# Kernel optimization log

Measured on AMD Instinct MI355X. Metric: run time of the kernel, lower is better.

## Reference

```python
import jax, jax.numpy as jnp
import numpy as np

B, T, D, H = 4, 1024, 512, 8
DK = D // H
P = 2 * T - 1  # relative position length


def rel_shift(x):
    # x: (b, h, t, 2t-1) -> (b, h, t, t), Transformer-XL relative shift
    b, h, t, p = x.shape
    x = jnp.pad(x, ((0, 0), (0, 0), (0, 0), (1, 0)))  # (b,h,t,p+1)
    x = x.reshape(b, h, p + 1, t)[:, :, 1:, :].reshape(b, h, t, p)
    return x[..., :t]


def setup_inputs() -> dict:
    key = jax.random.key(0)
    ks = jax.random.split(key, 16)
    s = 0.02
    return {
        "q": jax.random.normal(ks[0], (B, T, D), jnp.float32),
        "k": jax.random.normal(ks[1], (B, T, D), jnp.float32),
        "v": jax.random.normal(ks[2], (B, T, D), jnp.float32),
        "pos_emb": jax.random.normal(ks[3], (1, P, D), jnp.float32),
        "Wq": jax.random.normal(ks[4], (D, D), jnp.float32) * s,
        "bq": jnp.zeros((D,), jnp.float32),
        "Wk": jax.random.normal(ks[5], (D, D), jnp.float32) * s,
        "bk": jnp.zeros((D,), jnp.float32),
        "Wv": jax.random.normal(ks[6], (D, D), jnp.float32) * s,
        "bv": jnp.zeros((D,), jnp.float32),
        "Wp": jax.random.normal(ks[7], (D, D), jnp.float32) * s,
        "pos_bias_u": jax.random.normal(ks[8], (H, DK), jnp.float32) * s,
        "pos_bias_v": jax.random.normal(ks[9], (H, DK), jnp.float32) * s,
        "Wo": jax.random.normal(ks[10], (D, D), jnp.float32) * s,
        "bo": jnp.zeros((D,), jnp.float32),
    }


def reference(q, k, v, pos_emb, Wq, bq, Wk, bk, Wv, bv, Wp,
              pos_bias_u, pos_bias_v, Wo, bo):
    b, t, d = q.shape
    # QKV projections, split heads -> (b, t, h, dk)
    qh = (q @ Wq.T + bq).reshape(b, t, H, DK)
    kh = (k @ Wk.T + bk).reshape(b, t, H, DK)
    vh = (v @ Wv.T + bv).reshape(b, t, H, DK)
    # positional projection (no bias): (1, P, h, dk)
    ph = (pos_emb @ Wp.T).reshape(pos_emb.shape[1], H, DK)
    # content term: (q + u) . k
    q_u = qh + pos_bias_u  # (b,t,h,dk)
    matrix_ac = jnp.einsum("bqhd,bkhd->bhqk", q_u, kh)
    # position term: (q + v) . p, then relative shift
    q_v = qh + pos_bias_v
    matrix_bd = jnp.einsum("bqhd,phd->bhqp", q_v, ph)
    matrix_bd = rel_shift(matrix_bd)  # (b,h,t,t)
    scores = (matrix_ac + matrix_bd) / jnp.sqrt(jnp.float32(DK))
    attn = jax.nn.softmax(scores, axis=-1)
    out = jnp.einsum("bhqk,bkhd->bqhd", attn, vh).reshape(b, t, d)
    return out @ Wo.T + bo
```

## Files before the change

kernel.cpp:

```cpp
#include <hip/hip_runtime.h>
#include <math.h>

typedef unsigned short u16;
typedef _Float16 f16;
typedef __attribute__((ext_vector_type(8))) _Float16 f16x8;
typedef __attribute__((ext_vector_type(4))) float f32x4;

#define B_  4
#define T_  1024
#define D_  512
#define H_  8
#define DK_ 64
#define P_  2047

#define MFMAH(a, b, c) __builtin_amdgcn_mfma_f32_16x16x32_f16(a, b, c, 0, 0, 0)

__device__ __forceinline__ u16 f2hbits(float x) {
    union { f16 h; u16 u; } cv; cv.h = (f16)x; return cv.u;
}

__device__ __forceinline__ void gload_lds16(const u16* g, u16* l) {
    __builtin_amdgcn_global_load_lds(
        (const __attribute__((address_space(1))) void*)g,
        (__attribute__((address_space(3))) void*)l, 16, 0, 0);
}

__device__ __forceinline__ int swz8(int row, int colbase) {
    return row * 64 + (((colbase >> 3) ^ (row & 7)) << 3);
}

__global__ __launch_bounds__(256)
void conv_w(const float* __restrict__ wq, const float* __restrict__ wk,
            const float* __restrict__ wv, const float* __restrict__ wp,
            const float* __restrict__ wo,
            u16* wqs, u16* wks, u16* wvs, u16* wps, u16* wos)
{
    const int NW = 65536;
    int i = blockIdx.x * 256 + threadIdx.x;
    if (i >= 5 * NW) return;
    int which = i >> 16, off = i & (NW - 1);
    const float* src = which == 0 ? wq : which == 1 ? wk : which == 2 ? wv
                     : which == 3 ? wp : wo;
    u16* dst = which == 0 ? wqs : which == 1 ? wks : which == 2 ? wvs
             : which == 3 ? wps : wos;
    float4 x = *(const float4*)(src + (size_t)off * 4);
    union { f16 h[4]; uint2 u2; } cv;
    cv.h[0] = (f16)x.x; cv.h[1] = (f16)x.y;
    cv.h[2] = (f16)x.z; cv.h[3] = (f16)x.w;
    *(uint2*)(dst + (size_t)off * 4) = cv.u2;
}

__device__ __forceinline__ void gemm_core_f32(
    const float* __restrict__ A, const u16* __restrict__ Bw,
    int bm, int bn, int M, f32x4 (&acc)[4][4],
    u16 (&sA)[128][64], u16 (&sB)[128][64])
{
    const int tid = threadIdx.x;
    const int ln = tid & 63, w = tid >> 6;
    const int arow = ln & 15, kseg = ln >> 4;
    const int wr = w >> 1, wc = w & 1;

    for (int k0 = 0; k0 < 512; k0 += 64) {
        #pragma unroll
        for (int it = 0; it < 4; ++it) {
            int idx = it * 256 + tid;
            int r = idx >> 3, ch = idx & 7;
            int rm = bm + r; if (rm > M - 1) rm = M - 1;
            const float* s = A + (size_t)rm * 512 + k0 + ch * 8;
            float4 x = *(const float4*)s;
            float4 y = *(const float4*)(s + 4);
            union { f16 h[8]; f16x8 v; } pk;
            pk.h[0] = (f16)x.x; pk.h[1] = (f16)x.y;
            pk.h[2] = (f16)x.z; pk.h[3] = (f16)x.w;
            pk.h[4] = (f16)y.x; pk.h[5] = (f16)y.y;
            pk.h[6] = (f16)y.z; pk.h[7] = (f16)y.w;
            *(f16x8*)(&sA[r][(ch ^ (r & 7)) << 3]) = pk.v;
        }
        #pragma unroll
        for (int it = 0; it < 4; ++it) {
            int ch = it * 256 + tid;
            int r = ch >> 3, j = ch & 7;
            gload_lds16(Bw + (size_t)(bn + r) * 512 + k0 + ((j ^ (r & 7)) << 3),
                        &sB[0][0] + ch * 8);
        }
        __syncthreads();

        f16x8 af[4][2], bf[4][2];
        #pragma unroll
        for (int mi = 0; mi < 4; ++mi) {
            int row = wr * 64 + mi * 16 + arow;
            #pragma unroll
            for (int kc = 0; kc < 2; ++kc)
                af[mi][kc] = *(const f16x8*)
                    (&sA[row][0] + ((((kc << 2) | kseg) ^ (row & 7)) << 3));
        }
        #pragma unroll
        for (int nj = 0; nj < 4; ++nj) {
            int row = wc * 64 + nj * 16 + arow;
            #pragma unroll
            for (int kc = 0; kc < 2; ++kc)
                bf[nj][kc] = *(const f16x8*)
                    (&sB[row][0] + ((((kc << 2) | kseg) ^ (row & 7)) << 3));
        }
        #pragma unroll
        for (int mi = 0; mi < 4; ++mi)
            #pragma unroll
            for (int nj = 0; nj < 4; ++nj)
                #pragma unroll
                for (int kc = 0; kc < 2; ++kc)
                    acc[mi][nj] = MFMAH(af[mi][kc], bf[nj][kc], acc[mi][nj]);
        __syncthreads();
    }
}

__device__ __forceinline__ void gemm_core(
    const u16* __restrict__ A, const u16* __restrict__ Bw,
    int bm, int bn, int M, f32x4 (&acc)[4][4],
    u16 (&sA)[128][64], u16 (&sB)[128][64])
{
    const int tid = threadIdx.x;
    const int ln = tid & 63, w = tid >> 6;
    const int arow = ln & 15, kseg = ln >> 4;
    const int wr = w >> 1, wc = w & 1;

    for (int k0 = 0; k0 < 512; k0 += 64) {
        #pragma unroll
        for (int it = 0; it < 4; ++it) {
            int ch = it * 256 + tid;
            int r = ch >> 3, j = ch & 7;
            int rm = bm + r; if (rm > M - 1) rm = M - 1;
            gload_lds16(A + (size_t)rm * 512 + k0 + ((j ^ (r & 7)) << 3),
                        &sA[0][0] + ch * 8);
        }
        #pragma unroll
        for (int it = 0; it < 4; ++it) {
            int ch = it * 256 + tid;
            int r = ch >> 3, j = ch & 7;
            gload_lds16(Bw + (size_t)(bn + r) * 512 + k0 + ((j ^ (r & 7)) << 3),
                        &sB[0][0] + ch * 8);
        }
        __syncthreads();

        f16x8 af[4][2], bf[4][2];
        #pragma unroll
        for (int mi = 0; mi < 4; ++mi) {
            int row = wr * 64 + mi * 16 + arow;
            #pragma unroll
            for (int kc = 0; kc < 2; ++kc)
                af[mi][kc] = *(const f16x8*)
                    (&sA[row][0] + ((((kc << 2) | kseg) ^ (row & 7)) << 3));
        }
        #pragma unroll
        for (int nj = 0; nj < 4; ++nj) {
            int row = wc * 64 + nj * 16 + arow;
            #pragma unroll
            for (int kc = 0; kc < 2; ++kc)
                bf[nj][kc] = *(const f16x8*)
                    (&sB[row][0] + ((((kc << 2) | kseg) ^ (row & 7)) << 3));
        }
        #pragma unroll
        for (int mi = 0; mi < 4; ++mi)
            #pragma unroll
            for (int nj = 0; nj < 4; ++nj)
                #pragma unroll
                for (int kc = 0; kc < 2; ++kc)
                    acc[mi][nj] = MFMAH(af[mi][kc], bf[nj][kc], acc[mi][nj]);
        __syncthreads();
    }
}

__global__ __launch_bounds__(256, 3)
void gemm_qkvp(const float* __restrict__ q, const float* __restrict__ k,
               const float* __restrict__ v, const float* __restrict__ pe,
               const u16* __restrict__ wqs, const u16* __restrict__ wks,
               const u16* __restrict__ wvs, const u16* __restrict__ wps,
               const float* __restrict__ bq, const float* __restrict__ bk,
               const float* __restrict__ bv,
               const float* __restrict__ pbu, const float* __restrict__ pbv,
               u16* __restrict__ qub, u16* __restrict__ qvb,
               u16* __restrict__ kh, u16* __restrict__ vt, u16* __restrict__ ph)
{
    __shared__ u16 sA[128][64];
    __shared__ u16 sB[128][64];

    const int by = blockIdx.y;
    const float* A; const u16* Bw; const float* bias;
    int seg, bm, M, Tn;
    if (by < 32)      { seg=0; bm=by*128;       A=q;  Bw=wqs; bias=bq;      M=4096; Tn=T_; }
    else if (by < 64) { seg=1; bm=(by-32)*128;  A=k;  Bw=wks; bias=bk;      M=4096; Tn=T_; }
    else if (by < 96) { seg=2; bm=(by-64)*128;  A=v;  Bw=wvs; bias=bv;      M=4096; Tn=T_; }
    else              { seg=3; bm=(by-96)*128;  A=pe; Bw=wps; bias=nullptr; M=P_;   Tn=P_; }
    const int bn = blockIdx.x * 128;

    f32x4 acc[4][4] = {};
    gemm_core_f32(A, Bw, bm, bn, M, acc, sA, sB);

    const int tid = threadIdx.x;
    const int ln = tid & 63, w = tid >> 6;
    const int arow = ln & 15, kseg = ln >> 4;
    const int wr = w >> 1, wc = w & 1;

    float bv0[4];
    #pragma unroll
    for (int nj = 0; nj < 4; ++nj)
        bv0[nj] = bias ? bias[bn + wc * 64 + nj * 16 + arow] : 0.f;

    #pragma unroll
    for (int mi = 0; mi < 4; ++mi)
        #pragma unroll
        for (int r = 0; r < 4; ++r) {
            int m = bm + wr * 64 + mi * 16 + kseg * 4 + r;
            if (m >= M) continue;
            #pragma unroll
            for (int nj = 0; nj < 4; ++nj) {
                int n = bn + wc * 64 + nj * 16 + arow;
                float val = acc[mi][nj][r] + bv0[nj];
                if (seg == 0) {
                    int bb = m >> 10, t = m & 1023;
                    int hh = n >> 6, d = n & 63;
                    size_t off = ((size_t)(bb * H_ + hh) * T_ + t) * 64 + d;
                    qub[off] = f2hbits((val + pbu[hh * 64 + d]) * 0.125f);
                    qvb[off] = f2hbits((val + pbv[hh * 64 + d]) * 0.125f);
                } else if (seg == 2) {
                    int bb = m >> 10, t = m & 1023;
                    int hh = n >> 6, d = n & 63;
                    vt[((size_t)(bb * H_ + hh) * 64 + d) * T_ + t] = f2hbits(val);
                } else {
                    int bb = (Tn == T_) ? (m >> 10) : 0;
                    int t = m - bb * Tn;
                    int hh = n >> 6, d = n & 63;
                    size_t off = ((size_t)(bb * H_ + hh) * Tn + t) * 64 + d;
                    if (seg == 1) kh[off] = f2hbits(val);
                    else          ph[off] = f2hbits(val);
                }
            }
        }
}

__global__ __launch_bounds__(256, 3)
void gemm_out(const u16* __restrict__ A, const u16* __restrict__ Bw,
              const float* __restrict__ bias, float* __restrict__ C)
{
    __shared__ u16 sA[128][64];
    __shared__ u16 sB[128][64];
    const int bn = blockIdx.x * 128;
    const int bm = blockIdx.y * 128;
    f32x4 acc[4][4] = {};
    gemm_core(A, Bw, bm, bn, 4096, acc, sA, sB);

    const int tid = threadIdx.x;
    const int ln = tid & 63, w = tid >> 6;
    const int arow = ln & 15, kseg = ln >> 4;
    const int wr = w >> 1, wc = w & 1;
    #pragma unroll
    for (int mi = 0; mi < 4; ++mi)
        #pragma unroll
        for (int r = 0; r < 4; ++r) {
            int m = bm + wr * 64 + mi * 16 + kseg * 4 + r;
            #pragma unroll
            for (int nj = 0; nj < 4; ++nj) {
                int n = bn + wc * 64 + nj * 16 + arow;
                C[(size_t)m * 512 + n] = acc[mi][nj][r] + bias[n];
            }
        }
}

__global__ __launch_bounds__(256, 2)
void relattn_mfma(const u16* __restrict__ qub, const u16* __restrict__ qvb,
                  const u16* __restrict__ kh, const u16* __restrict__ vt,
                  const u16* __restrict__ ph,
                  u16* __restrict__ ao)
{
    __shared__ u16 s_k[3][64][64];
    __shared__ u16 s_p[3][64][64];
    __shared__ u16 s_pp[4][16][64];

    const int tid = threadIdx.x;
    const int ln  = tid & 63;
    const int w   = tid >> 6;
    const int arow = ln & 15;
    const int kseg = ln >> 4;

    const int lg = ((blockIdx.x & 7) << 6) | (blockIdx.x >> 3);
    const int qt = lg & 15, h = (lg >> 4) & 7, b = lg >> 7;
    const int q0 = qt * 64;

    const size_t kvbase = (size_t)(b * H_ + h) * T_ * 64;
    const size_t vtbase = (size_t)(b * H_ + h) * 64 * T_;
    const size_t pbase  = (size_t)h * P_ * 64;
    const int jb0 = 960 - q0;

    f16x8 qu[2], qv[2];
    {
        const u16* qb = qub + kvbase + (size_t)(q0 + w * 16 + arow) * 64;
        const u16* vb = qvb + kvbase + (size_t)(q0 + w * 16 + arow) * 64;
        #pragma unroll
        for (int c = 0; c < 2; ++c) {
            qu[c] = *(const f16x8*)(qb + c * 32 + kseg * 8);
            qv[c] = *(const f16x8*)(vb + c * 32 + kseg * 8);
        }
    }

    f32x4 o_[4] = {};
    float l_run[4] = {};

    auto stage_k = [&](int kt, int slot) {
        #pragma unroll
        for (int it = 0; it < 2; ++it) {
            int idx = tid + it * 256;
            int r = idx >> 3, ch = idx & 7;
            const u16* src = kh + kvbase + (size_t)(kt * 64 + r) * 64 + ((ch ^ (r & 7)) << 3);
            gload_lds16(src, &s_k[slot][0][0] + idx * 8);
        }
    };
    auto stage_p = [&](int c, int slot) {
        #pragma unroll
        for (int it = 0; it < 2; ++it) {
            int idx = tid + it * 256;
            int r = idx >> 3, ch = idx & 7;
            int j = jb0 + c * 64 + r; if (j > P_ - 1) j = P_ - 1;
            const u16* src = ph + pbase + (size_t)j * 64 + ((ch ^ (r & 7)) << 3);
            gload_lds16(src, &s_p[slot][0][0] + idx * 8);
        }
    };
    auto bd_chunk = [&](int slot, f32x4* out) {
        #pragma unroll
        for (int nb = 0; nb < 4; ++nb) {
            int pr = nb * 16 + arow;
            f16x8 b0 = *(const f16x8*)(&s_p[slot][0][0] + swz8(pr, kseg * 8));
            f16x8 b1 = *(const f16x8*)(&s_p[slot][0][0] + swz8(pr, 32 + kseg * 8));
            out[nb] = MFMAH(qv[0], b0, out[nb]);
            out[nb] = MFMAH(qv[1], b1, out[nb]);
        }
    };

    stage_k(0, 0); stage_k(1, 1);
    stage_p(0, 0); stage_p(1, 1); stage_p(2, 2);
    __syncthreads();
    f32x4 carry[4] = {};
    bd_chunk(0, carry);
    asm volatile("" ::: "memory");
    __builtin_amdgcn_s_barrier();
    asm volatile("" ::: "memory");

    int ks = 0;
    for (int t = 0; t < 16; ++t) {
        const int k0 = t * 64;
        const int pr = (ks + 1 > 2) ? 0 : ks + 1;
        const int kw = (ks + 2 > 2) ? ks - 1 : ks + 2;

        f16x8 vfr[4][2];
        #pragma unroll
        for (int nt = 0; nt < 4; ++nt) {
            const u16* vp = vt + vtbase + (size_t)(nt * 16 + arow) * T_ + k0 + kseg * 8;
            vfr[nt][0] = *(const f16x8*)vp;
            vfr[nt][1] = *(const f16x8*)(vp + 32);
        }

        if (t < 14) { stage_k(t + 2, kw); stage_p(t + 3, ks); }

        __builtin_amdgcn_s_setprio(1);
        f32x4 ac[4] = {};
        #pragma unroll
        for (int nt = 0; nt < 4; ++nt) {
            int kr = nt * 16 + arow;
            f16x8 b0 = *(const f16x8*)(&s_k[ks][0][0] + swz8(kr, kseg * 8));
            f16x8 b1 = *(const f16x8*)(&s_k[ks][0][0] + swz8(kr, 32 + kseg * 8));
            ac[nt] = MFMAH(qu[0], b0, ac[nt]);
            ac[nt] = MFMAH(qu[1], b1, ac[nt]);
        }
        f32x4 bdn[4] = {};
        bd_chunk(pr, bdn);
        __builtin_amdgcn_s_setprio(0);

        float win[5][4];
        #pragma unroll
        for (int r = 0; r < 4; ++r) {
            if (w == 0)      { win[0][r]=carry[3][r]; win[1][r]=bdn[0][r];   win[2][r]=bdn[1][r];   win[3][r]=bdn[2][r];   win[4][r]=bdn[3][r]; }
            else if (w == 1) { win[0][r]=carry[2][r]; win[1][r]=carry[3][r]; win[2][r]=bdn[0][r];   win[3][r]=bdn[1][r];   win[4][r]=bdn[2][r]; }
            else if (w == 2) { win[0][r]=carry[1][r]; win[1][r]=carry[2][r]; win[2][r]=carry[3][r]; win[3][r]=bdn[0][r];   win[4][r]=bdn[1][r]; }
            else             { win[0][r]=carry[0][r]; win[1][r]=carry[1][r]; win[2][r]=carry[2][r]; win[3][r]=carry[3][r]; win[4][r]=bdn[0][r]; }
        }

        #pragma unroll
        for (int r = 0; r < 4; ++r) {
            int sl  = 15 - (kseg << 2) - r;
            int src = (ln & 48) | ((arow + sl) & 15);
            bool hi = (arow < sl);
            int r16 = kseg * 4 + r;
            #pragma unroll
            for (int nt = 0; nt < 4; ++nt) {
                float sel = hi ? win[nt + 1][r] : win[nt][r];
                float pm = __shfl(sel, src, 64);
                float pv = __expf(ac[nt][r] + pm);
                l_run[r] += pv;
                int kl = nt * 16 + arow;
                s_pp[w][r16][(((kl >> 3) ^ (r16 & 7)) << 3) | (kl & 7)] = f2hbits(pv);
            }
        }
        asm volatile("s_waitcnt lgkmcnt(0)" ::: "memory");
        __builtin_amdgcn_sched_barrier(0);

        f16x8 pa0 = *(const f16x8*)(&s_pp[w][arow][0] + ((kseg ^ (arow & 7)) << 3));
        f16x8 pa1 = *(const f16x8*)(&s_pp[w][arow][0] + (((4 + kseg) ^ (arow & 7)) << 3));
        __builtin_amdgcn_s_setprio(1);
        #pragma unroll
        for (int nt = 0; nt < 4; ++nt) {
            o_[nt] = MFMAH(pa0, vfr[nt][0], o_[nt]);
            o_[nt] = MFMAH(pa1, vfr[nt][1], o_[nt]);
        }
        __builtin_amdgcn_s_setprio(0);

        #pragma unroll
        for (int nb = 0; nb < 4; ++nb) carry[nb] = bdn[nb];

        asm volatile("" ::: "memory");
        __builtin_amdgcn_s_barrier();
        asm volatile("" ::: "memory");
        ks = pr;
    }

    #pragma unroll
    for (int r = 0; r < 4; ++r) {
        float l = l_run[r];
        l += __shfl_xor(l, 1); l += __shfl_xor(l, 2);
        l += __shfl_xor(l, 4); l += __shfl_xor(l, 8);
        l_run[r] = 1.f / l;
    }
    #pragma unroll
    for (int nt = 0; nt < 4; ++nt)
        #pragma unroll
        for (int r = 0; r < 4; ++r) {
            int qrow = q0 + w * 16 + kseg * 4 + r;
            size_t off = ((size_t)(b * T_ + qrow)) * D_ + h * DK_ + nt * 16 + arow;
            ao[off] = f2hbits(o_[nt][r] * l_run[r]);
        }
}

extern "C" void kernel_launch(void* const* d_in, const int* in_sizes, int n_in,
                              void* d_out, int out_size, void* d_ws, size_t ws_size,
                              hipStream_t stream)
{
    const float* q   = (const float*)d_in[0];
    const float* k   = (const float*)d_in[1];
    const float* v   = (const float*)d_in[2];
    const float* pe  = (const float*)d_in[3];
    const float* Wq  = (const float*)d_in[4];
    const float* bq  = (const float*)d_in[5];
    const float* Wk  = (const float*)d_in[6];
    const float* bk  = (const float*)d_in[7];
    const float* Wv  = (const float*)d_in[8];
    const float* bv  = (const float*)d_in[9];
    const float* Wp  = (const float*)d_in[10];
    const float* pbu = (const float*)d_in[11];
    const float* pbv = (const float*)d_in[12];
    const float* Wo  = (const float*)d_in[13];
    const float* bo  = (const float*)d_in[14];
    float* out = (float*)d_out;

    char* ws = (char*)d_ws;
    const size_t MB = 1024 * 1024;
    const size_t HMB = 512 * 1024;
    u16* wqs = (u16*)(ws);
    u16* wks = (u16*)(ws + 1 * HMB);
    u16* wvs = (u16*)(ws + 2 * HMB);
    u16* wps = (u16*)(ws + 3 * HMB);
    u16* wos = (u16*)(ws + 4 * HMB);
    u16* qub = (u16*)(ws + 3 * MB);
    u16* qvb = (u16*)(ws + 7 * MB);
    u16* kh  = (u16*)(ws + 11 * MB);
    u16* vt  = (u16*)(ws + 15 * MB);
    u16* ph  = (u16*)(ws + 19 * MB);
    u16* ao  = (u16*)(ws + 22 * MB);

    dim3 blk(256);
    conv_w<<<dim3(1280), blk, 0, stream>>>(Wq, Wk, Wv, Wp, Wo,
                                           wqs, wks, wvs, wps, wos);

    gemm_qkvp<<<dim3(4, 112), blk, 0, stream>>>(
        q, k, v, pe, wqs, wks, wvs, wps,
        bq, bk, bv, pbu, pbv, qub, qvb, kh, vt, ph);

    relattn_mfma<<<dim3(512), blk, 0, stream>>>(qub, qvb, kh, vt, ph, ao);

    gemm_out<<<dim3(4, 32), blk, 0, stream>>>(ao, wos, bo, out);
}
```

Baseline: 93.05 us.

## Double-buffer LDS in projection GEMMs to overlap global loads with MFMA

Both GEMM cores switch to two LDS buffers so the next k-tile's global loads (register-staged fp32 A with f16 conversion, or direct-to-LDS for f16 operands) are issued before the current tile's MFMAs. Explicit waitcnt and s_barrier calls replace __syncthreads, and s_setprio raises wave priority around the MFMA block. This targets load latency stalls in the QKV/pos and output projections. It doubles LDS per block and lowers the launch-bounds occupancy hint from 3 to 2 blocks, and the hand-placed waitcnt counts must match the number of outstanding loads.

```diff
diff --git a/kernel.cpp b/kernel.cpp
--- a/kernel.cpp
+++ b/kernel.cpp
@@ -50,40 +50,64 @@
     *(uint2*)(dst + (size_t)off * 4) = cv.u2;
 }
 
-__device__ __forceinline__ void gemm_core_f32(
+__device__ __forceinline__ void gemm_core_f32a(
     const float* __restrict__ A, const u16* __restrict__ Bw,
     int bm, int bn, int M, f32x4 (&acc)[4][4],
-    u16 (&sA)[128][64], u16 (&sB)[128][64])
+    u16 (&sA)[2][128][64], u16 (&sB)[2][128][64])
 {
     const int tid = threadIdx.x;
     const int ln = tid & 63, w = tid >> 6;
     const int arow = ln & 15, kseg = ln >> 4;
     const int wr = w >> 1, wc = w & 1;
 
-    for (int k0 = 0; k0 < 512; k0 += 64) {
-        #pragma unroll
-        for (int it = 0; it < 4; ++it) {
-            int idx = it * 256 + tid;
+    float4 a0[4], a1[4];
+
+    auto issueA = [&](int k0) {
+        #pragma unroll
+        for (int g = 0; g < 4; ++g) {
+            int idx = g * 256 + tid;
             int r = idx >> 3, ch = idx & 7;
             int rm = bm + r; if (rm > M - 1) rm = M - 1;
             const float* s = A + (size_t)rm * 512 + k0 + ch * 8;
-            float4 x = *(const float4*)s;
-            float4 y = *(const float4*)(s + 4);
+            a0[g] = *(const float4*)s;
+            a1[g] = *(const float4*)(s + 4);
+        }
+    };
+    auto writeA = [&](int buf) {
+        #pragma unroll
+        for (int g = 0; g < 4; ++g) {
+            int idx = g * 256 + tid;
+            int r = idx >> 3, ch = idx & 7;
             union { f16 h[8]; f16x8 v; } pk;
-            pk.h[0] = (f16)x.x; pk.h[1] = (f16)x.y;
-            pk.h[2] = (f16)x.z; pk.h[3] = (f16)x.w;
-            pk.h[4] = (f16)y.x; pk.h[5] = (f16)y.y;
-            pk.h[6] = (f16)y.z; pk.h[7] = (f16)y.w;
-            *(f16x8*)(&sA[r][(ch ^ (r & 7)) << 3]) = pk.v;
-        }
+            pk.h[0] = (f16)a0[g].x; pk.h[1] = (f16)a0[g].y;
+            pk.h[2] = (f16)a0[g].z; pk.h[3] = (f16)a0[g].w;
+            pk.h[4] = (f16)a1[g].x; pk.h[5] = (f16)a1[g].y;
+            pk.h[6] = (f16)a1[g].z; pk.h[7] = (f16)a1[g].w;
+            *(f16x8*)(&sA[buf][r][(ch ^ (r & 7)) << 3]) = pk.v;
+        }
+    };
+    auto issueB = [&](int k0, int buf) {
         #pragma unroll
         for (int it = 0; it < 4; ++it) {
             int ch = it * 256 + tid;
             int r = ch >> 3, j = ch & 7;
             gload_lds16(Bw + (size_t)(bn + r) * 512 + k0 + ((j ^ (r & 7)) << 3),
-                        &sB[0][0] + ch * 8);
-        }
-        __syncthreads();
+                        &sB[buf][0][0] + ch * 8);
+        }
+    };
+
+    issueA(0);
+    issueB(0, 0);
+    for (int t = 0; t < 8; ++t) {
+        const int cur = t & 1;
+        asm volatile("s_waitcnt vmcnt(0)" ::: "memory");
+        writeA(cur);
+        if (t < 7) issueA((t + 1) * 64);
+        asm volatile("s_waitcnt lgkmcnt(0)" ::: "memory");
+        __builtin_amdgcn_sched_barrier(0);
+        __builtin_amdgcn_s_barrier();
+        asm volatile("" ::: "memory");
+        if (t < 7) issueB((t + 1) * 64, cur ^ 1);
 
         f16x8 af[4][2], bf[4][2];
         #pragma unroll
@@ -92,7 +116,7 @@
             #pragma unroll
             for (int kc = 0; kc < 2; ++kc)
                 af[mi][kc] = *(const f16x8*)
-                    (&sA[row][0] + ((((kc << 2) | kseg) ^ (row & 7)) << 3));
+                    (&sA[cur][row][0] + ((((kc << 2) | kseg) ^ (row & 7)) << 3));
         }
         #pragma unroll
         for (int nj = 0; nj < 4; ++nj) {
@@ -100,8 +124,9 @@
             #pragma unroll
             for (int kc = 0; kc < 2; ++kc)
                 bf[nj][kc] = *(const f16x8*)
-                    (&sB[row][0] + ((((kc << 2) | kseg) ^ (row & 7)) << 3));
-        }
+                    (&sB[cur][row][0] + ((((kc << 2) | kseg) ^ (row & 7)) << 3));
+        }
+        __builtin_amdgcn_s_setprio(1);
         #pragma unroll
         for (int mi = 0; mi < 4; ++mi)
             #pragma unroll
@@ -109,37 +134,50 @@
                 #pragma unroll
                 for (int kc = 0; kc < 2; ++kc)
                     acc[mi][nj] = MFMAH(af[mi][kc], bf[nj][kc], acc[mi][nj]);
-        __syncthreads();
+        __builtin_amdgcn_s_setprio(0);
+        asm volatile("" ::: "memory");
     }
 }
 
 __device__ __forceinline__ void gemm_core(
     const u16* __restrict__ A, const u16* __restrict__ Bw,
     int bm, int bn, int M, f32x4 (&acc)[4][4],
-    u16 (&sA)[128][64], u16 (&sB)[128][64])
+    u16 (&sA)[2][128][64], u16 (&sB)[2][128][64])
 {
     const int tid = threadIdx.x;
     const int ln = tid & 63, w = tid >> 6;
     const int arow = ln & 15, kseg = ln >> 4;
     const int wr = w >> 1, wc = w & 1;
 
-    for (int k0 = 0; k0 < 512; k0 += 64) {
+    auto stage = [&](int k0, int buf) {
         #pragma unroll
         for (int it = 0; it < 4; ++it) {
             int ch = it * 256 + tid;
             int r = ch >> 3, j = ch & 7;
             int rm = bm + r; if (rm > M - 1) rm = M - 1;
             gload_lds16(A + (size_t)rm * 512 + k0 + ((j ^ (r & 7)) << 3),
-                        &sA[0][0] + ch * 8);
+                        &sA[buf][0][0] + ch * 8);
         }
         #pragma unroll
         for (int it = 0; it < 4; ++it) {
             int ch = it * 256 + tid;
             int r = ch >> 3, j = ch & 7;
             gload_lds16(Bw + (size_t)(bn + r) * 512 + k0 + ((j ^ (r & 7)) << 3),
-                        &sB[0][0] + ch * 8);
-        }
-        __syncthreads();
+                        &sB[buf][0][0] + ch * 8);
+        }
+    };
+
+    stage(0, 0);
+    for (int t = 0; t < 8; ++t) {
+        const int cur = t & 1;
+        if (t < 7) {
+            stage((t + 1) * 64, cur ^ 1);
+            asm volatile("s_waitcnt vmcnt(8)" ::: "memory");
+        } else {
+            asm volatile("s_waitcnt vmcnt(0)" ::: "memory");
+        }
+        __builtin_amdgcn_sched_barrier(0);
+        __builtin_amdgcn_s_barrier();
 
         f16x8 af[4][2], bf[4][2];
         #pragma unroll
@@ -148,7 +186,7 @@
             #pragma unroll
             for (int kc = 0; kc < 2; ++kc)
                 af[mi][kc] = *(const f16x8*)
-                    (&sA[row][0] + ((((kc << 2) | kseg) ^ (row & 7)) << 3));
+                    (&sA[cur][row][0] + ((((kc << 2) | kseg) ^ (row & 7)) << 3));
         }
         #pragma unroll
         for (int nj = 0; nj < 4; ++nj) {
@@ -156,8 +194,9 @@
             #pragma unroll
             for (int kc = 0; kc < 2; ++kc)
                 bf[nj][kc] = *(const f16x8*)
-                    (&sB[row][0] + ((((kc << 2) | kseg) ^ (row & 7)) << 3));
-        }
+                    (&sB[cur][row][0] + ((((kc << 2) | kseg) ^ (row & 7)) << 3));
+        }
+        __builtin_amdgcn_s_setprio(1);
         #pragma unroll
         for (int mi = 0; mi < 4; ++mi)
             #pragma unroll
@@ -165,11 +204,15 @@
                 #pragma unroll
                 for (int kc = 0; kc < 2; ++kc)
                     acc[mi][nj] = MFMAH(af[mi][kc], bf[nj][kc], acc[mi][nj]);
-        __syncthreads();
+        __builtin_amdgcn_s_setprio(0);
+
+        asm volatile("" ::: "memory");
+        __builtin_amdgcn_s_barrier();
+        asm volatile("" ::: "memory");
     }
 }
 
-__global__ __launch_bounds__(256, 3)
+__global__ __launch_bounds__(256, 2)
 void gemm_qkvp(const float* __restrict__ q, const float* __restrict__ k,
                const float* __restrict__ v, const float* __restrict__ pe,
                const u16* __restrict__ wqs, const u16* __restrict__ wks,
@@ -180,8 +223,8 @@
                u16* __restrict__ qub, u16* __restrict__ qvb,
                u16* __restrict__ kh, u16* __restrict__ vt, u16* __restrict__ ph)
 {
-    __shared__ u16 sA[128][64];
-    __shared__ u16 sB[128][64];
+    __shared__ u16 sA[2][128][64];
+    __shared__ u16 sB[2][128][64];
 
     const int by = blockIdx.y;
     const float* A; const u16* Bw; const float* bias;
@@ -193,7 +236,7 @@
     const int bn = blockIdx.x * 128;
 
     f32x4 acc[4][4] = {};
-    gemm_core_f32(A, Bw, bm, bn, M, acc, sA, sB);
+    gemm_core_f32a(A, Bw, bm, bn, M, acc, sA, sB);
 
     const int tid = threadIdx.x;
     const int ln = tid & 63, w = tid >> 6;
@@ -237,12 +280,12 @@
         }
 }
 
-__global__ __launch_bounds__(256, 3)
+__global__ __launch_bounds__(256, 2)
 void gemm_out(const u16* __restrict__ A, const u16* __restrict__ Bw,
               const float* __restrict__ bias, float* __restrict__ C)
 {
-    __shared__ u16 sA[128][64];
-    __shared__ u16 sB[128][64];
+    __shared__ u16 sA[2][128][64];
+    __shared__ u16 sB[2][128][64];
     const int bn = blockIdx.x * 128;
     const int bm = blockIdx.y * 128;
     f32x4 acc[4][4] = {};
```

Result: no change. 91.32 us (-1.9%).
